# Optimization experiments

Measured on AMD Instinct MI355X. Metric: run time of the kernel, lower is better.

## Reference

```python
import jax, jax.numpy as jnp
import numpy as np

B, S, H, NH = 4, 2048, 1024, 16
HD = H // NH
EPS = 1e-12


def setup_inputs() -> dict:
    key = jax.random.key(0)
    ks = jax.random.split(key, 12)
    sc = 0.02
    return {
        "query": jax.random.normal(ks[0], (B, S, H), dtype=jnp.float32),
        "attention_mask": jnp.zeros((B, 1, 1, S), dtype=jnp.float32),
        "Wq": jax.random.normal(ks[1], (H, H), dtype=jnp.float32) * sc,
        "bq": jnp.zeros((H,), dtype=jnp.float32),
        "Wk": jax.random.normal(ks[2], (H, H), dtype=jnp.float32) * sc,
        "bk": jnp.zeros((H,), dtype=jnp.float32),
        "Wv": jax.random.normal(ks[3], (H, H), dtype=jnp.float32) * sc,
        "bv": jnp.zeros((H,), dtype=jnp.float32),
        "Wd": jax.random.normal(ks[4], (H, H), dtype=jnp.float32) * sc,
        "bd": jnp.zeros((H,), dtype=jnp.float32),
        "ln_gamma": jnp.ones((H,), dtype=jnp.float32),
        "ln_beta": jnp.zeros((H,), dtype=jnp.float32),
    }


def reference(query, attention_mask, Wq, bq, Wk, bk, Wv, bv, Wd, bd, ln_gamma, ln_beta):
    # QKV projections: [B,S,H] -> [B,S,NH,HD]
    q = (query @ Wq + bq).reshape(B, S, NH, HD)
    k = (query @ Wk + bk).reshape(B, S, NH, HD)
    v = (query @ Wv + bv).reshape(B, S, NH, HD)
    # scores: [B,NH,S,S]
    scores = jnp.einsum("bqhd,bkhd->bhqk", q, k) / jnp.sqrt(jnp.float32(HD))
    scores = scores + attention_mask
    probs = jax.nn.softmax(scores, axis=-1)  # attn_dropout p=0 (eval)
    ctx = jnp.einsum("bhqk,bkhd->bqhd", probs, v).reshape(B, S, H)
    hidden = ctx @ Wd + bd  # out_dropout p=0 (eval)
    # pre-LN residual path: LN(hidden) + query
    mu = jnp.mean(hidden, axis=-1, keepdims=True)
    var = jnp.mean(jnp.square(hidden - mu), axis=-1, keepdims=True)
    hidden = (hidden - mu) * jax.lax.rsqrt(var + EPS) * ln_gamma + ln_beta
    return hidden + query
```

## Files before the change

kernel.cpp:

```cpp
#include <hip/hip_runtime.h>
#include <stdint.h>

#define Bn 4
#define Sn 2048
#define Hn 1024
#define NHn 16
#define Mn 8192

typedef unsigned short bf_t;
typedef __attribute__((ext_vector_type(8))) short s16x8;
typedef __attribute__((ext_vector_type(4))) short s16x4;
typedef __attribute__((ext_vector_type(8))) unsigned short u16x8;
typedef __attribute__((ext_vector_type(4))) unsigned short u16x4;
typedef __attribute__((ext_vector_type(4))) float f32x4;
typedef __attribute__((ext_vector_type(4))) unsigned int u32x4;
typedef __attribute__((ext_vector_type(2))) unsigned int u32x2;

__device__ __forceinline__ bf_t f2bf(float f) {
  unsigned int u = __float_as_uint(f);
  u += 0x7fffu + ((u >> 16) & 1u);
  return (bf_t)(u >> 16);
}

__device__ __forceinline__ unsigned pk2(float lo, float hi) {
  return __builtin_amdgcn_perm(__float_as_uint(hi), __float_as_uint(lo), 0x07060302u);
}
__device__ __forceinline__ s16x4 pack4(float a0, float a1, float a2, float a3) {
  u32x2 t;
  t[0] = pk2(a0, a1);
  t[1] = pk2(a2, a3);
  return __builtin_bit_cast(s16x4, t);
}

#define MFMA16K16(a, b, c) __builtin_amdgcn_mfma_f32_16x16x16bf16_1k(a, b, c, 0, 0, 0)
#define MFMA32(a, b, c) __builtin_amdgcn_mfma_f32_16x16x32_bf16(a, b, c, 0, 0, 0)

#define GLOAD16(gp, lp) __builtin_amdgcn_global_load_lds(              \
    (__attribute__((address_space(1))) void*)(gp),                     \
    (__attribute__((address_space(3))) void*)(lp), 16, 0, 0)

__global__ __launch_bounds__(256)
void prep(const float* __restrict__ Wq, const float* __restrict__ Wk,
          const float* __restrict__ Wv, const float* __restrict__ Wd,
          const float* __restrict__ query,
          bf_t* __restrict__ Wt, bf_t* __restrict__ Wdt, bf_t* __restrict__ Xb) {
  __shared__ float tile[32][33];
  const int z = blockIdx.z;
  const int tx = threadIdx.x;
  const int ty = threadIdx.y;
  if (z == 4) {
    const int bid = blockIdx.y * 32 + blockIdx.x;
    const int t = ty * 32 + tx;
    const size_t base = (size_t)bid * 8192 + t * 4;
#pragma unroll
    for (int i = 0; i < 8; i++) {
      const f32x4 v = *(const f32x4*)(query + base + i * 1024);
      u16x4 o;
      o[0] = f2bf(v[0]); o[1] = f2bf(v[1]); o[2] = f2bf(v[2]); o[3] = f2bf(v[3]);
      *(u16x4*)(Xb + base + i * 1024) = o;
    }
    return;
  }
  const float* W = (z == 0) ? Wq : (z == 1) ? Wk : (z == 2) ? Wv : Wd;
  bf_t* dst = (z < 3) ? Wt + (size_t)z * Hn * Hn : Wdt;
  const int n0 = blockIdx.x * 32, k0 = blockIdx.y * 32;
#pragma unroll
  for (int i = 0; i < 4; i++)
    tile[ty + i * 8][tx] = W[(size_t)(k0 + ty + i * 8) * Hn + n0 + tx];
  __syncthreads();
#pragma unroll
  for (int i = 0; i < 4; i++) {
    const int nn = ty + i * 8, kk = tx;
    dst[(size_t)(n0 + nn) * Hn + k0 + kk] = f2bf(tile[kk][nn]);
  }
}

__global__ __launch_bounds__(256, 3)
void gemm_bt(const bf_t* __restrict__ A, const bf_t* __restrict__ Bt,
             const float* __restrict__ b0, const float* __restrict__ b1,
             const float* __restrict__ b2, void* __restrict__ outp,
             int N, int K, int out_bf16)
{
  __shared__ bf_t As[2][4096];
  __shared__ bf_t Bs[2][4096];
  const int tid = threadIdx.x;
  const int wave = tid >> 6, lane = tid & 63;
  const int l15 = lane & 15, quad = lane >> 4;
  const int bm = blockIdx.y * 128, bn = blockIdx.x * 128;
  const int wm = (wave >> 1) * 64, wn = (wave & 1) * 64;
  const int srow = tid >> 2;
  const int scol = (tid & 3) * 8;

  const bf_t* Ag = A + (size_t)(bm + srow) * K + scol;
  const bf_t* Bg = Bt + (size_t)(bn + srow) * K + scol;

  f32x4 acc[4][4] = {};

  GLOAD16(Ag, As[0] + tid * 8);
  GLOAD16(Ag + (size_t)64 * K, As[0] + 2048 + tid * 8);
  GLOAD16(Bg, Bs[0] + tid * 8);
  GLOAD16(Bg + (size_t)64 * K, Bs[0] + 2048 + tid * 8);

  const int nIter = K >> 5;
  for (int i = 0; i < nIter; i++) {
    const int cur = i & 1;
    __syncthreads();
    if (i + 1 < nIter) {
      const int k0 = (i + 1) * 32;
      GLOAD16(Ag + k0, As[cur ^ 1] + tid * 8);
      GLOAD16(Ag + (size_t)64 * K + k0, As[cur ^ 1] + 2048 + tid * 8);
      GLOAD16(Bg + k0, Bs[cur ^ 1] + tid * 8);
      GLOAD16(Bg + (size_t)64 * K + k0, Bs[cur ^ 1] + 2048 + tid * 8);
    }
    s16x8 af[4], bfr[4];
#pragma unroll
    for (int mi = 0; mi < 4; mi++)
      af[mi] = *(const s16x8*)&As[cur][(wm + mi * 16 + l15) * 32 + quad * 8];
#pragma unroll
    for (int ni = 0; ni < 4; ni++)
      bfr[ni] = *(const s16x8*)&Bs[cur][(wn + ni * 16 + l15) * 32 + quad * 8];
#pragma unroll
    for (int mi = 0; mi < 4; mi++)
#pragma unroll
      for (int ni = 0; ni < 4; ni++)
        acc[mi][ni] = __builtin_amdgcn_mfma_f32_16x16x32_bf16(af[mi], bfr[ni], acc[mi][ni], 0, 0, 0);
  }

#pragma unroll
  for (int ni = 0; ni < 4; ni++) {
    const int gn = bn + wn + ni * 16 + l15;
    const float* bp = (gn < 1024) ? b0 : ((gn < 2048) ? b1 : b2);
    const float bias = bp[gn & 1023];
#pragma unroll
    for (int mi = 0; mi < 4; mi++) {
#pragma unroll
      for (int r = 0; r < 4; r++) {
        const int gm = bm + wm + mi * 16 + quad * 4 + r;
        const float v = acc[mi][ni][r] + bias;
        if (out_bf16) ((bf_t*)outp)[(size_t)gm * N + gn] = f2bf(v);
        else          ((float*)outp)[(size_t)gm * N + gn] = v;
      }
    }
  }
}

__global__ __launch_bounds__(256)
void kvswz(const bf_t* __restrict__ qkv, bf_t* __restrict__ Kf,
           bf_t* __restrict__ Vf, const float* __restrict__ mask,
           bf_t* __restrict__ Fb) {
  __shared__ u32x4 smbuf[640];
  const int t = threadIdx.x;
  const int bh = blockIdx.y, b = bh >> 4, h = bh & 15;
  const int k0 = blockIdx.x * 64;

  if (blockIdx.z == 0) {
    bf_t* KT = (bf_t*)smbuf;
#pragma unroll
    for (int i = 0; i < 2; i++) {
      const int c = t + i * 256;
      const int row = c >> 3, col8 = (c & 7) * 8;
      const u16x8 v = *(const u16x8*)(qkv + (size_t)(b * Sn + k0 + row) * 3072 + 1024 + h * 64 + col8);
      *(u16x8*)&KT[row * 80 + col8] = v;
    }
    __syncthreads();
    bf_t* dst0 = Kf + ((size_t)(bh * 32 + blockIdx.x) * 8) * 512;
#pragma unroll
    for (int i = 0; i < 2; i++) {
      const int p = t + i * 256;
      const int frag = p >> 6, lane = p & 63;
      const int ks = frag >> 1, half = frag & 1;
      const int l15 = lane & 15, quad = lane >> 4;
      const u16x8 v = *(const u16x8*)&KT[(ks * 16 + l15) * 80 + half * 32 + quad * 8];
      *(u16x8*)(dst0 + (size_t)frag * 512 + lane * 8) = v;
    }
  } else {
    unsigned int* P32 = (unsigned int*)smbuf;
    {
      const int kp = t >> 3;
      const int d0 = (t & 7) * 8;
      const int kg = k0 + 2 * kp;
      const float f0 = __builtin_amdgcn_exp2f(mask[b * Sn + kg] * 1.44269504f);
      const float f1 = __builtin_amdgcn_exp2f(mask[b * Sn + kg + 1] * 1.44269504f);
      const bf_t* p0 = qkv + (size_t)(b * Sn + kg) * 3072 + 2048 + h * 64 + d0;
      const u16x8 r0 = *(const u16x8*)p0;
      const u16x8 r1 = *(const u16x8*)(p0 + 3072);
#pragma unroll
      for (int j = 0; j < 8; j++) {
        const float v0 = __uint_as_float((unsigned)r0[j] << 16) * f0;
        const float v1 = __uint_as_float((unsigned)r1[j] << 16) * f1;
        P32[(d0 + j) * 33 + kp] = pk2(v0, v1);
      }
    }
    if (h == 0 && t < 64) {
      const float fm = __builtin_amdgcn_exp2f(mask[b * Sn + k0 + t] * 1.44269504f);
      Fb[b * Sn + k0 + t] = f2bf(fm);
    }
    __syncthreads();
    bf_t* dst0 = Vf + ((size_t)(bh * 32 + blockIdx.x) * 8) * 512;
#pragma unroll
    for (int i = 0; i < 2; i++) {
      const int p = t + i * 256;
      const int fp = p >> 6, lane = p & 63;
      const int dvblk = fp >> 1, kpair = fp & 1;
      const int l15 = lane & 15, quad = (lane >> 4) & 3;
      const int d = dvblk * 16 + l15;
      const int c = kpair * 16 + quad * 2;
      u32x4 w;
      w[0] = P32[d * 33 + c];
      w[1] = P32[d * 33 + c + 1];
      w[2] = P32[d * 33 + c + 8];
      w[3] = P32[d * 33 + c + 9];
      *(u32x4*)(dst0 + (size_t)(kpair * 4 + dvblk) * 512 + lane * 8) = w;
    }
  }
}

__global__ __launch_bounds__(512)
void attn(const bf_t* __restrict__ qkv, const bf_t* __restrict__ Kf,
          const bf_t* __restrict__ Vf, const bf_t* __restrict__ Fb,
          bf_t* __restrict__ ctx)
{
  __shared__ __align__(16) bf_t KV[2][2][2][2048];
  __shared__ __align__(16) bf_t Fs[2048];

  const int tid = threadIdx.x;
  const int wave = tid >> 6, lane = tid & 63;
  const int g = wave >> 2, wv = wave & 3;
  const int tg = tid & 255;
  const int l15 = lane & 15, quad = lane >> 4;
  const int idx = blockIdx.x;
  const int bh = idx & 63, b = bh >> 4, h = bh & 15;
  const int q0 = (idx >> 6) * 128;

  if (tid < 256) GLOAD16(Fb + (size_t)b * Sn + tid * 8, Fs + tid * 8);

  s16x8 aq[2][2];
#pragma unroll
  for (int qf = 0; qf < 2; qf++) {
    const bf_t* qp = qkv + (size_t)(b * Sn + q0 + wv * 32 + qf * 16 + l15) * 3072 + h * 64;
    aq[qf][0] = *(const s16x8*)(qp + quad * 8);
    aq[qf][1] = *(const s16x8*)(qp + 32 + quad * 8);
  }

  f32x4 lacc[2] = {};
  f32x4 o[2][4] = {};

  const bf_t* kb = Kf + (size_t)bh * 131072 + (size_t)g * 65536;
  const bf_t* vb = Vf + (size_t)bh * 131072 + (size_t)g * 65536;
  const float C1 = 0.125f * 1.44269504f;

  GLOAD16(kb + tg * 8, KV[g][0][0] + tg * 8);
  GLOAD16(vb + tg * 8, KV[g][1][0] + tg * 8);

  for (int it = 0; it < 32; ++it) {
    const int cur = it & 1;
    __syncthreads();
    if (it < 31) {
      GLOAD16(kb + (it + 1) * 2048 + tg * 8, KV[g][0][cur ^ 1] + tg * 8);
      GLOAD16(vb + (it + 1) * 2048 + tg * 8, KV[g][1][cur ^ 1] + tg * 8);
    }

    s16x4 pb[2][2];
#pragma unroll
    for (int e = 0; e < 2; e++) {
      const s16x8 k0f = *(const s16x8*)&KV[g][0][cur][(e * 2 + 0) * 512 + lane * 8];
      const s16x8 k1f = *(const s16x8*)&KV[g][0][cur][(e * 2 + 1) * 512 + lane * 8];
      const s16x4 ff = *(const s16x4*)&Fs[g * 1024 + it * 32 + e * 16 + quad * 4];
#pragma unroll
      for (int qf = 0; qf < 2; qf++) {
        f32x4 acc = {};
        __builtin_amdgcn_s_setprio(1);
        acc = MFMA32(k0f, aq[qf][0], acc);
        acc = MFMA32(k1f, aq[qf][1], acc);
        __builtin_amdgcn_s_setprio(0);
        const float p0 = __builtin_amdgcn_exp2f(acc[0] * C1);
        const float p1 = __builtin_amdgcn_exp2f(acc[1] * C1);
        const float p2 = __builtin_amdgcn_exp2f(acc[2] * C1);
        const float p3 = __builtin_amdgcn_exp2f(acc[3] * C1);
        pb[qf][e] = pack4(p0, p1, p2, p3);
        lacc[qf] = MFMA16K16(ff, pb[qf][e], lacc[qf]);
      }
    }

    __builtin_amdgcn_s_setprio(1);
#pragma unroll
    for (int dvblk = 0; dvblk < 4; dvblk++) {
      const s16x8 vv = *(const s16x8*)&KV[g][1][cur][dvblk * 512 + lane * 8];
      const s16x4 vlo = {vv[0], vv[1], vv[2], vv[3]};
      const s16x4 vhi = {vv[4], vv[5], vv[6], vv[7]};
#pragma unroll
      for (int qf = 0; qf < 2; qf++) {
        o[qf][dvblk] = MFMA16K16(vlo, pb[qf][0], o[qf][dvblk]);
        o[qf][dvblk] = MFMA16K16(vhi, pb[qf][1], o[qf][dvblk]);
      }
    }
    __builtin_amdgcn_s_setprio(0);
  }

  __syncthreads();
  float* sm = (float*)&KV[0][0][0][0];
  float* sl = (float*)&Fs[0];
  if (g == 1) {
#pragma unroll
    for (int qf = 0; qf < 2; qf++) {
      const int row = wv * 32 + qf * 16 + l15;
#pragma unroll
      for (int dvblk = 0; dvblk < 4; dvblk++) {
        const int col = (dvblk * 16 + quad * 4 + l15 * 4) & 63;
        *(f32x4*)&sm[row * 64 + col] = o[qf][dvblk];
      }
      if (quad == 0) sl[row] = lacc[qf][0];
    }
  }
  __syncthreads();
  if (g == 0) {
#pragma unroll
    for (int qf = 0; qf < 2; qf++) {
      const int row = wv * 32 + qf * 16 + l15;
      const float inv = 1.f / (lacc[qf][0] + sl[row]);
      const size_t grow = (size_t)(b * Sn + q0 + row);
#pragma unroll
      for (int dvblk = 0; dvblk < 4; dvblk++) {
        const int col = (dvblk * 16 + quad * 4 + l15 * 4) & 63;
        const f32x4 o2 = *(const f32x4*)&sm[row * 64 + col];
        u16x4 ov;
#pragma unroll
        for (int r = 0; r < 4; r++) ov[r] = f2bf((o[qf][dvblk][r] + o2[r]) * inv);
        *(u16x4*)&ctx[grow * Hn + h * 64 + dvblk * 16 + quad * 4] = ov;
      }
    }
  }
}

__global__ __launch_bounds__(256)
void ln_res(const float* __restrict__ hid, const float* __restrict__ query,
            const float* __restrict__ gamma, const float* __restrict__ beta,
            float* __restrict__ out)
{
  const int row = blockIdx.x, t = threadIdx.x;
  const f32x4 h = *(const f32x4*)(hid + (size_t)row * Hn + t * 4);
  float s = h[0] + h[1] + h[2] + h[3];
  float ss = h[0]*h[0] + h[1]*h[1] + h[2]*h[2] + h[3]*h[3];
#pragma unroll
  for (int m = 32; m; m >>= 1) { s += __shfl_xor(s, m); ss += __shfl_xor(ss, m); }
  __shared__ float red[8];
  if ((t & 63) == 0) { red[t >> 6] = s; red[4 + (t >> 6)] = ss; }
  __syncthreads();
  s = red[0] + red[1] + red[2] + red[3];
  ss = red[4] + red[5] + red[6] + red[7];
  const float mu = s * (1.f / Hn);
  const float rs = rsqrtf(ss * (1.f / Hn) - mu * mu + 1e-12f);
  const f32x4 q = *(const f32x4*)(query + (size_t)row * Hn + t * 4);
  const f32x4 g = *(const f32x4*)(gamma + t * 4);
  const f32x4 be = *(const f32x4*)(beta + t * 4);
  f32x4 o;
#pragma unroll
  for (int j = 0; j < 4; j++) o[j] = (h[j] - mu) * rs * g[j] + be[j] + q[j];
  *(f32x4*)(out + (size_t)row * Hn + t * 4) = o;
}

extern "C" void kernel_launch(void* const* d_in, const int* in_sizes, int n_in,
                              void* d_out, int out_size, void* d_ws, size_t ws_size,
                              hipStream_t stream) {
  const float* query = (const float*)d_in[0];
  const float* mask  = (const float*)d_in[1];
  const float* Wq = (const float*)d_in[2];
  const float* bq = (const float*)d_in[3];
  const float* Wk = (const float*)d_in[4];
  const float* bk = (const float*)d_in[5];
  const float* Wv = (const float*)d_in[6];
  const float* bv = (const float*)d_in[7];
  const float* Wd = (const float*)d_in[8];
  const float* bd = (const float*)d_in[9];
  const float* gamma = (const float*)d_in[10];
  const float* beta  = (const float*)d_in[11];

  char* w = (char*)d_ws;
  bf_t* Xb  = (bf_t*)w;  w += (size_t)Mn * Hn * 2;
  bf_t* Wt  = (bf_t*)w;  w += (size_t)3 * Hn * Hn * 2;
  bf_t* Wdt = (bf_t*)w;  w += (size_t)Hn * Hn * 2;
  bf_t* QKV = (bf_t*)w;  w += (size_t)Mn * 3 * Hn * 2;
  bf_t* Vf  = (bf_t*)w;  w += (size_t)64 * 32 * 4096 * 2;
  bf_t* Ctx = (bf_t*)w;  w += (size_t)Mn * Hn * 2;
  bf_t* Kf  = (bf_t*)w;
  float* Hid = (float*)w;  w += (size_t)Mn * Hn * 4;
  bf_t* Fb = (bf_t*)w;

  prep<<<dim3(32, 32, 5), dim3(32, 8), 0, stream>>>(Wq, Wk, Wv, Wd, query, Wt, Wdt, Xb);
  gemm_bt<<<dim3(24, 64), 256, 0, stream>>>(Xb, Wt, bq, bk, bv, QKV, 3072, 1024, 1);
  kvswz<<<dim3(32, 64, 2), 256, 0, stream>>>(QKV, Kf, Vf, mask, Fb);
  attn<<<1024, 512, 0, stream>>>(QKV, Kf, Vf, Fb, Ctx);
  gemm_bt<<<dim3(8, 64), 256, 0, stream>>>(Ctx, Wdt, bd, bd, bd, Hid, 1024, 1024, 0);
  ln_res<<<Mn, 256, 0, stream>>>(Hid, query, gamma, beta, (float*)d_out);
}
```

Measured before the change: 331.8 us.

## Load K fragments directly from QKV and double query rows per attention block

```diff
diff --git a/kernel.cpp b/kernel.cpp
--- a/kernel.cpp
+++ b/kernel.cpp
@@ -145,80 +145,55 @@
 }
 
 __global__ __launch_bounds__(256)
-void kvswz(const bf_t* __restrict__ qkv, bf_t* __restrict__ Kf,
-           bf_t* __restrict__ Vf, const float* __restrict__ mask,
-           bf_t* __restrict__ Fb) {
-  __shared__ u32x4 smbuf[640];
+void kvswz(const bf_t* __restrict__ qkv, bf_t* __restrict__ Vf,
+           const float* __restrict__ mask, bf_t* __restrict__ Fb) {
+  __shared__ unsigned int P32[64 * 33];
   const int t = threadIdx.x;
   const int bh = blockIdx.y, b = bh >> 4, h = bh & 15;
   const int k0 = blockIdx.x * 64;
 
-  if (blockIdx.z == 0) {
-    bf_t* KT = (bf_t*)smbuf;
-#pragma unroll
-    for (int i = 0; i < 2; i++) {
-      const int c = t + i * 256;
-      const int row = c >> 3, col8 = (c & 7) * 8;
-      const u16x8 v = *(const u16x8*)(qkv + (size_t)(b * Sn + k0 + row) * 3072 + 1024 + h * 64 + col8);
-      *(u16x8*)&KT[row * 80 + col8] = v;
-    }
-    __syncthreads();
-    bf_t* dst0 = Kf + ((size_t)(bh * 32 + blockIdx.x) * 8) * 512;
-#pragma unroll
-    for (int i = 0; i < 2; i++) {
-      const int p = t + i * 256;
-      const int frag = p >> 6, lane = p & 63;
-      const int ks = frag >> 1, half = frag & 1;
-      const int l15 = lane & 15, quad = lane >> 4;
-      const u16x8 v = *(const u16x8*)&KT[(ks * 16 + l15) * 80 + half * 32 + quad * 8];
-      *(u16x8*)(dst0 + (size_t)frag * 512 + lane * 8) = v;
-    }
-  } else {
-    unsigned int* P32 = (unsigned int*)smbuf;
-    {
-      const int kp = t >> 3;
-      const int d0 = (t & 7) * 8;
-      const int kg = k0 + 2 * kp;
-      const float f0 = __builtin_amdgcn_exp2f(mask[b * Sn + kg] * 1.44269504f);
-      const float f1 = __builtin_amdgcn_exp2f(mask[b * Sn + kg + 1] * 1.44269504f);
-      const bf_t* p0 = qkv + (size_t)(b * Sn + kg) * 3072 + 2048 + h * 64 + d0;
-      const u16x8 r0 = *(const u16x8*)p0;
-      const u16x8 r1 = *(const u16x8*)(p0 + 3072);
-#pragma unroll
-      for (int j = 0; j < 8; j++) {
-        const float v0 = __uint_as_float((unsigned)r0[j] << 16) * f0;
-        const float v1 = __uint_as_float((unsigned)r1[j] << 16) * f1;
-        P32[(d0 + j) * 33 + kp] = pk2(v0, v1);
-      }
-    }
-    if (h == 0 && t < 64) {
-      const float fm = __builtin_amdgcn_exp2f(mask[b * Sn + k0 + t] * 1.44269504f);
-      Fb[b * Sn + k0 + t] = f2bf(fm);
-    }
-    __syncthreads();
-    bf_t* dst0 = Vf + ((size_t)(bh * 32 + blockIdx.x) * 8) * 512;
-#pragma unroll
-    for (int i = 0; i < 2; i++) {
-      const int p = t + i * 256;
-      const int fp = p >> 6, lane = p & 63;
-      const int dvblk = fp >> 1, kpair = fp & 1;
-      const int l15 = lane & 15, quad = (lane >> 4) & 3;
-      const int d = dvblk * 16 + l15;
-      const int c = kpair * 16 + quad * 2;
-      u32x4 w;
-      w[0] = P32[d * 33 + c];
-      w[1] = P32[d * 33 + c + 1];
-      w[2] = P32[d * 33 + c + 8];
-      w[3] = P32[d * 33 + c + 9];
-      *(u32x4*)(dst0 + (size_t)(kpair * 4 + dvblk) * 512 + lane * 8) = w;
-    }
+  {
+    const int kp = t >> 3;
+    const int d0 = (t & 7) * 8;
+    const int kg = k0 + 2 * kp;
+    const float f0 = __builtin_amdgcn_exp2f(mask[b * Sn + kg] * 1.44269504f);
+    const float f1 = __builtin_amdgcn_exp2f(mask[b * Sn + kg + 1] * 1.44269504f);
+    const bf_t* p0 = qkv + (size_t)(b * Sn + kg) * 3072 + 2048 + h * 64 + d0;
+    const u16x8 r0 = *(const u16x8*)p0;
+    const u16x8 r1 = *(const u16x8*)(p0 + 3072);
+#pragma unroll
+    for (int j = 0; j < 8; j++) {
+      const float v0 = __uint_as_float((unsigned)r0[j] << 16) * f0;
+      const float v1 = __uint_as_float((unsigned)r1[j] << 16) * f1;
+      P32[(d0 + j) * 33 + kp] = pk2(v0, v1);
+    }
+  }
+  if (h == 0 && t < 64) {
+    const float fm = __builtin_amdgcn_exp2f(mask[b * Sn + k0 + t] * 1.44269504f);
+    Fb[b * Sn + k0 + t] = f2bf(fm);
+  }
+  __syncthreads();
+  bf_t* dst0 = Vf + ((size_t)(bh * 32 + blockIdx.x) * 8) * 512;
+#pragma unroll
+  for (int i = 0; i < 2; i++) {
+    const int p = t + i * 256;
+    const int fp = p >> 6, lane = p & 63;
+    const int dvblk = fp >> 1, kpair = fp & 1;
+    const int l15 = lane & 15, quad = (lane >> 4) & 3;
+    const int d = dvblk * 16 + l15;
+    const int c = kpair * 16 + quad * 2;
+    u32x4 w;
+    w[0] = P32[d * 33 + c];
+    w[1] = P32[d * 33 + c + 1];
+    w[2] = P32[d * 33 + c + 8];
+    w[3] = P32[d * 33 + c + 9];
+    *(u32x4*)(dst0 + (size_t)(kpair * 4 + dvblk) * 512 + lane * 8) = w;
   }
 }
 
 __global__ __launch_bounds__(512)
-void attn(const bf_t* __restrict__ qkv, const bf_t* __restrict__ Kf,
-          const bf_t* __restrict__ Vf, const bf_t* __restrict__ Fb,
-          bf_t* __restrict__ ctx)
+void attn(const bf_t* __restrict__ qkv, const bf_t* __restrict__ Vf,
+          const bf_t* __restrict__ Fb, bf_t* __restrict__ ctx)
 {
   __shared__ __align__(16) bf_t KV[2][2][2][2048];
   __shared__ __align__(16) bf_t Fs[2048];
@@ -230,44 +205,47 @@
   const int l15 = lane & 15, quad = lane >> 4;
   const int idx = blockIdx.x;
   const int bh = idx & 63, b = bh >> 4, h = bh & 15;
-  const int q0 = (idx >> 6) * 128;
+  const int q0 = (idx >> 6) * 256;
 
   if (tid < 256) GLOAD16(Fb + (size_t)b * Sn + tid * 8, Fs + tid * 8);
 
-  s16x8 aq[2][2];
-#pragma unroll
-  for (int qf = 0; qf < 2; qf++) {
-    const bf_t* qp = qkv + (size_t)(b * Sn + q0 + wv * 32 + qf * 16 + l15) * 3072 + h * 64;
+  s16x8 aq[4][2];
+#pragma unroll
+  for (int qf = 0; qf < 4; qf++) {
+    const bf_t* qp = qkv + (size_t)(b * Sn + q0 + wv * 64 + qf * 16 + l15) * 3072 + h * 64;
     aq[qf][0] = *(const s16x8*)(qp + quad * 8);
     aq[qf][1] = *(const s16x8*)(qp + 32 + quad * 8);
   }
 
-  f32x4 lacc[2] = {};
-  f32x4 o[2][4] = {};
-
-  const bf_t* kb = Kf + (size_t)bh * 131072 + (size_t)g * 65536;
+  f32x4 lacc[4] = {};
+  f32x4 o[4][4] = {};
+
+  const int ks = tg >> 7, kh = (tg >> 6) & 1;
+  const int lg = tg & 63, l15g = lg & 15, quadg = lg >> 4;
+  const bf_t* kq = qkv + (size_t)(b * Sn + g * 1024 + ks * 16 + l15g) * 3072
+                   + 1024 + h * 64 + kh * 32 + quadg * 8;
   const bf_t* vb = Vf + (size_t)bh * 131072 + (size_t)g * 65536;
   const float C1 = 0.125f * 1.44269504f;
 
-  GLOAD16(kb + tg * 8, KV[g][0][0] + tg * 8);
+  GLOAD16(kq, KV[g][0][0] + tg * 8);
   GLOAD16(vb + tg * 8, KV[g][1][0] + tg * 8);
 
   for (int it = 0; it < 32; ++it) {
     const int cur = it & 1;
     __syncthreads();
     if (it < 31) {
-      GLOAD16(kb + (it + 1) * 2048 + tg * 8, KV[g][0][cur ^ 1] + tg * 8);
+      GLOAD16(kq + (size_t)(it + 1) * 98304, KV[g][0][cur ^ 1] + tg * 8);
       GLOAD16(vb + (it + 1) * 2048 + tg * 8, KV[g][1][cur ^ 1] + tg * 8);
     }
 
-    s16x4 pb[2][2];
+    s16x4 pb[4][2];
 #pragma unroll
     for (int e = 0; e < 2; e++) {
       const s16x8 k0f = *(const s16x8*)&KV[g][0][cur][(e * 2 + 0) * 512 + lane * 8];
       const s16x8 k1f = *(const s16x8*)&KV[g][0][cur][(e * 2 + 1) * 512 + lane * 8];
       const s16x4 ff = *(const s16x4*)&Fs[g * 1024 + it * 32 + e * 16 + quad * 4];
 #pragma unroll
-      for (int qf = 0; qf < 2; qf++) {
+      for (int qf = 0; qf < 4; qf++) {
         f32x4 acc = {};
         __builtin_amdgcn_s_setprio(1);
         acc = MFMA32(k0f, aq[qf][0], acc);
@@ -289,7 +267,7 @@
       const s16x4 vlo = {vv[0], vv[1], vv[2], vv[3]};
       const s16x4 vhi = {vv[4], vv[5], vv[6], vv[7]};
 #pragma unroll
-      for (int qf = 0; qf < 2; qf++) {
+      for (int qf = 0; qf < 4; qf++) {
         o[qf][dvblk] = MFMA16K16(vlo, pb[qf][0], o[qf][dvblk]);
         o[qf][dvblk] = MFMA16K16(vhi, pb[qf][1], o[qf][dvblk]);
       }
@@ -297,36 +275,41 @@
     __builtin_amdgcn_s_setprio(0);
   }
 
-  __syncthreads();
   float* sm = (float*)&KV[0][0][0][0];
   float* sl = (float*)&Fs[0];
-  if (g == 1) {
-#pragma unroll
-    for (int qf = 0; qf < 2; qf++) {
-      const int row = wv * 32 + qf * 16 + l15;
-#pragma unroll
-      for (int dvblk = 0; dvblk < 4; dvblk++) {
-        const int col = (dvblk * 16 + quad * 4 + l15 * 4) & 63;
-        *(f32x4*)&sm[row * 64 + col] = o[qf][dvblk];
-      }
-      if (quad == 0) sl[row] = lacc[qf][0];
-    }
-  }
-  __syncthreads();
-  if (g == 0) {
-#pragma unroll
-    for (int qf = 0; qf < 2; qf++) {
-      const int row = wv * 32 + qf * 16 + l15;
-      const float inv = 1.f / (lacc[qf][0] + sl[row]);
-      const size_t grow = (size_t)(b * Sn + q0 + row);
-#pragma unroll
-      for (int dvblk = 0; dvblk < 4; dvblk++) {
-        const int col = (dvblk * 16 + quad * 4 + l15 * 4) & 63;
-        const f32x4 o2 = *(const f32x4*)&sm[row * 64 + col];
-        u16x4 ov;
-#pragma unroll
-        for (int r = 0; r < 4; r++) ov[r] = f2bf((o[qf][dvblk][r] + o2[r]) * inv);
-        *(u16x4*)&ctx[grow * Hn + h * 64 + dvblk * 16 + quad * 4] = ov;
+#pragma unroll
+  for (int qh = 0; qh < 2; qh++) {
+    __syncthreads();
+    if (g == 1) {
+#pragma unroll
+      for (int lq = 0; lq < 2; lq++) {
+        const int qf = qh * 2 + lq;
+        const int rp = wv * 32 + lq * 16 + l15;
+#pragma unroll
+        for (int dvblk = 0; dvblk < 4; dvblk++) {
+          const int col = (dvblk * 16 + quad * 4 + l15 * 4) & 63;
+          *(f32x4*)&sm[rp * 64 + col] = o[qf][dvblk];
+        }
+        if (quad == 0) sl[rp] = lacc[qf][0];
+      }
+    }
+    __syncthreads();
+    if (g == 0) {
+#pragma unroll
+      for (int lq = 0; lq < 2; lq++) {
+        const int qf = qh * 2 + lq;
+        const int rp = wv * 32 + lq * 16 + l15;
+        const float inv = 1.f / (lacc[qf][0] + sl[rp]);
+        const size_t grow = (size_t)(b * Sn + q0 + wv * 64 + qf * 16 + l15);
+#pragma unroll
+        for (int dvblk = 0; dvblk < 4; dvblk++) {
+          const int col = (dvblk * 16 + quad * 4 + l15 * 4) & 63;
+          const f32x4 o2 = *(const f32x4*)&sm[rp * 64 + col];
+          u16x4 ov;
+#pragma unroll
+          for (int r = 0; r < 4; r++) ov[r] = f2bf((o[qf][dvblk][r] + o2[r]) * inv);
+          *(u16x4*)&ctx[grow * Hn + h * 64 + dvblk * 16 + quad * 4] = ov;
+        }
       }
     }
   }
@@ -382,14 +365,13 @@
   bf_t* QKV = (bf_t*)w;  w += (size_t)Mn * 3 * Hn * 2;
   bf_t* Vf  = (bf_t*)w;  w += (size_t)64 * 32 * 4096 * 2;
   bf_t* Ctx = (bf_t*)w;  w += (size_t)Mn * Hn * 2;
-  bf_t* Kf  = (bf_t*)w;
   float* Hid = (float*)w;  w += (size_t)Mn * Hn * 4;
   bf_t* Fb = (bf_t*)w;
 
   prep<<<dim3(32, 32, 5), dim3(32, 8), 0, stream>>>(Wq, Wk, Wv, Wd, query, Wt, Wdt, Xb);
   gemm_bt<<<dim3(24, 64), 256, 0, stream>>>(Xb, Wt, bq, bk, bv, QKV, 3072, 1024, 1);
-  kvswz<<<dim3(32, 64, 2), 256, 0, stream>>>(QKV, Kf, Vf, mask, Fb);
-  attn<<<1024, 512, 0, stream>>>(QKV, Kf, Vf, Fb, Ctx);
+  kvswz<<<dim3(32, 64), 256, 0, stream>>>(QKV, Vf, mask, Fb);
+  attn<<<512, 512, 0, stream>>>(QKV, Vf, Fb, Ctx);
   gemm_bt<<<dim3(8, 64), 256, 0, stream>>>(Ctx, Wdt, bd, bd, bd, Hid, 1024, 1024, 0);
   ln_res<<<Mn, 256, 0, stream>>>(Hid, query, gamma, beta, (float*)d_out);
 }
```

New measurement: 357.0 us. 7.6% more time.

## Double attention block to 256 queries and remap GEMM workgroups across XCDs

Applied to the files above, without the earlier changes.

```diff
diff --git a/kernel.cpp b/kernel.cpp
--- a/kernel.cpp
+++ b/kernel.cpp
@@ -86,7 +86,14 @@
   const int tid = threadIdx.x;
   const int wave = tid >> 6, lane = tid & 63;
   const int l15 = lane & 15, quad = lane >> 4;
-  const int bm = blockIdx.y * 128, bn = blockIdx.x * 128;
+
+  const int nwg = gridDim.x * gridDim.y;
+  const int lin = blockIdx.y * gridDim.x + blockIdx.x;
+  const int qc = nwg >> 3;
+  const int wg = (lin & 7) * qc + (lin >> 3);
+  const int bxs = wg % gridDim.x, bys = wg / gridDim.x;
+  const int bm = bys * 128, bn = bxs * 128;
+
   const int wm = (wave >> 1) * 64, wn = (wave & 1) * 64;
   const int srow = tid >> 2;
   const int scol = (tid & 3) * 8;
@@ -215,7 +222,7 @@
   }
 }
 
-__global__ __launch_bounds__(512)
+__global__ __launch_bounds__(1024)
 void attn(const bf_t* __restrict__ qkv, const bf_t* __restrict__ Kf,
           const bf_t* __restrict__ Vf, const bf_t* __restrict__ Fb,
           bf_t* __restrict__ ctx)
@@ -225,12 +232,12 @@
 
   const int tid = threadIdx.x;
   const int wave = tid >> 6, lane = tid & 63;
-  const int g = wave >> 2, wv = wave & 3;
-  const int tg = tid & 255;
+  const int g = wave >> 3, wv = wave & 7;
+  const int tg = tid & 511;
   const int l15 = lane & 15, quad = lane >> 4;
   const int idx = blockIdx.x;
   const int bh = idx & 63, b = bh >> 4, h = bh & 15;
-  const int q0 = (idx >> 6) * 128;
+  const int q0 = (idx >> 6) * 256;
 
   if (tid < 256) GLOAD16(Fb + (size_t)b * Sn + tid * 8, Fs + tid * 8);
 
@@ -249,15 +256,17 @@
   const bf_t* vb = Vf + (size_t)bh * 131072 + (size_t)g * 65536;
   const float C1 = 0.125f * 1.44269504f;
 
-  GLOAD16(kb + tg * 8, KV[g][0][0] + tg * 8);
-  GLOAD16(vb + tg * 8, KV[g][1][0] + tg * 8);
+  if (tg < 256) GLOAD16(kb + tg * 8, KV[g][0][0] + tg * 8);
+  else          GLOAD16(vb + (tg - 256) * 8, KV[g][1][0] + (tg - 256) * 8);
 
   for (int it = 0; it < 32; ++it) {
     const int cur = it & 1;
     __syncthreads();
     if (it < 31) {
-      GLOAD16(kb + (it + 1) * 2048 + tg * 8, KV[g][0][cur ^ 1] + tg * 8);
-      GLOAD16(vb + (it + 1) * 2048 + tg * 8, KV[g][1][cur ^ 1] + tg * 8);
+      if (tg < 256)
+        GLOAD16(kb + (it + 1) * 2048 + tg * 8, KV[g][0][cur ^ 1] + tg * 8);
+      else
+        GLOAD16(vb + (it + 1) * 2048 + (tg - 256) * 8, KV[g][1][cur ^ 1] + (tg - 256) * 8);
     }
 
     s16x4 pb[2][2];
@@ -297,36 +306,39 @@
     __builtin_amdgcn_s_setprio(0);
   }
 
-  __syncthreads();
   float* sm = (float*)&KV[0][0][0][0];
   float* sl = (float*)&Fs[0];
-  if (g == 1) {
-#pragma unroll
-    for (int qf = 0; qf < 2; qf++) {
-      const int row = wv * 32 + qf * 16 + l15;
-#pragma unroll
-      for (int dvblk = 0; dvblk < 4; dvblk++) {
-        const int col = (dvblk * 16 + quad * 4 + l15 * 4) & 63;
-        *(f32x4*)&sm[row * 64 + col] = o[qf][dvblk];
-      }
-      if (quad == 0) sl[row] = lacc[qf][0];
-    }
-  }
-  __syncthreads();
-  if (g == 0) {
-#pragma unroll
-    for (int qf = 0; qf < 2; qf++) {
-      const int row = wv * 32 + qf * 16 + l15;
-      const float inv = 1.f / (lacc[qf][0] + sl[row]);
-      const size_t grow = (size_t)(b * Sn + q0 + row);
-#pragma unroll
-      for (int dvblk = 0; dvblk < 4; dvblk++) {
-        const int col = (dvblk * 16 + quad * 4 + l15 * 4) & 63;
-        const f32x4 o2 = *(const f32x4*)&sm[row * 64 + col];
-        u16x4 ov;
-#pragma unroll
-        for (int r = 0; r < 4; r++) ov[r] = f2bf((o[qf][dvblk][r] + o2[r]) * inv);
-        *(u16x4*)&ctx[grow * Hn + h * 64 + dvblk * 16 + quad * 4] = ov;
+#pragma unroll
+  for (int ph = 0; ph < 2; ph++) {
+    __syncthreads();
+    if (g == 1 && (wv >> 2) == ph) {
+#pragma unroll
+      for (int qf = 0; qf < 2; qf++) {
+        const int rp = (wv & 3) * 32 + qf * 16 + l15;
+#pragma unroll
+        for (int dvblk = 0; dvblk < 4; dvblk++) {
+          const int col = (dvblk * 16 + quad * 4 + l15 * 4) & 63;
+          *(f32x4*)&sm[rp * 64 + col] = o[qf][dvblk];
+        }
+        if (quad == 0) sl[rp] = lacc[qf][0];
+      }
+    }
+    __syncthreads();
+    if (g == 0 && (wv >> 2) == ph) {
+#pragma unroll
+      for (int qf = 0; qf < 2; qf++) {
+        const int rp = (wv & 3) * 32 + qf * 16 + l15;
+        const float inv = 1.f / (lacc[qf][0] + sl[rp]);
+        const size_t grow = (size_t)(b * Sn + q0 + wv * 32 + qf * 16 + l15);
+#pragma unroll
+        for (int dvblk = 0; dvblk < 4; dvblk++) {
+          const int col = (dvblk * 16 + quad * 4 + l15 * 4) & 63;
+          const f32x4 o2 = *(const f32x4*)&sm[rp * 64 + col];
+          u16x4 ov;
+#pragma unroll
+          for (int r = 0; r < 4; r++) ov[r] = f2bf((o[qf][dvblk][r] + o2[r]) * inv);
+          *(u16x4*)&ctx[grow * Hn + h * 64 + dvblk * 16 + quad * 4] = ov;
+        }
       }
     }
   }
@@ -389,7 +401,7 @@
   prep<<<dim3(32, 32, 5), dim3(32, 8), 0, stream>>>(Wq, Wk, Wv, Wd, query, Wt, Wdt, Xb);
   gemm_bt<<<dim3(24, 64), 256, 0, stream>>>(Xb, Wt, bq, bk, bv, QKV, 3072, 1024, 1);
   kvswz<<<dim3(32, 64, 2), 256, 0, stream>>>(QKV, Kf, Vf, mask, Fb);
-  attn<<<1024, 512, 0, stream>>>(QKV, Kf, Vf, Fb, Ctx);
+  attn<<<512, 1024, 0, stream>>>(QKV, Kf, Vf, Fb, Ctx);
   gemm_bt<<<dim3(8, 64), 256, 0, stream>>>(Ctx, Wdt, bd, bd, bd, Hid, 1024, 1024, 0);
   ln_res<<<Mn, 256, 0, stream>>>(Hid, query, gamma, beta, (float*)d_out);
 }
```

After: 328.8 us. Within noise of the previous version (-0.9%).

## Fuse K/V swizzle into QKV GEMM epilogue and remap workgroups

Applied to the files above, without the earlier changes.

```diff
diff --git a/kernel.cpp b/kernel.cpp
--- a/kernel.cpp
+++ b/kernel.cpp
@@ -42,8 +42,9 @@
 __global__ __launch_bounds__(256)
 void prep(const float* __restrict__ Wq, const float* __restrict__ Wk,
           const float* __restrict__ Wv, const float* __restrict__ Wd,
-          const float* __restrict__ query,
-          bf_t* __restrict__ Wt, bf_t* __restrict__ Wdt, bf_t* __restrict__ Xb) {
+          const float* __restrict__ query, const float* __restrict__ mask,
+          bf_t* __restrict__ Wt, bf_t* __restrict__ Wdt, bf_t* __restrict__ Xb,
+          bf_t* __restrict__ Fb) {
   __shared__ float tile[32][33];
   const int z = blockIdx.z;
   const int tx = threadIdx.x;
@@ -59,6 +60,13 @@
       o[0] = f2bf(v[0]); o[1] = f2bf(v[1]); o[2] = f2bf(v[2]); o[3] = f2bf(v[3]);
       *(u16x4*)(Xb + base + i * 1024) = o;
     }
+    if (bid < 4) {
+#pragma unroll
+      for (int i = 0; i < 8; i++) {
+        const int s = t * 8 + i;
+        Fb[bid * Sn + s] = f2bf(__builtin_amdgcn_exp2f(mask[(size_t)bid * Sn + s] * 1.44269504f));
+      }
+    }
     return;
   }
   const float* W = (z == 0) ? Wq : (z == 1) ? Wk : (z == 2) ? Wv : Wd;
@@ -79,14 +87,25 @@
 void gemm_bt(const bf_t* __restrict__ A, const bf_t* __restrict__ Bt,
              const float* __restrict__ b0, const float* __restrict__ b1,
              const float* __restrict__ b2, void* __restrict__ outp,
-             int N, int K, int out_bf16)
+             int N, int K, int out_bf16,
+             const float* __restrict__ mask, bf_t* __restrict__ Kf,
+             bf_t* __restrict__ Vf, int fuse_kv)
 {
-  __shared__ bf_t As[2][4096];
-  __shared__ bf_t Bs[2][4096];
+  __shared__ __align__(16) char smem[33536];
+  bf_t (*As)[4096] = (bf_t(*)[4096])smem;
+  bf_t (*Bs)[4096] = (bf_t(*)[4096])(smem + 16384);
+
   const int tid = threadIdx.x;
   const int wave = tid >> 6, lane = tid & 63;
   const int l15 = lane & 15, quad = lane >> 4;
-  const int bm = blockIdx.y * 128, bn = blockIdx.x * 128;
+
+  const int nwg = gridDim.x * gridDim.y;
+  const int lin = blockIdx.y * gridDim.x + blockIdx.x;
+  const int qc = nwg >> 3;
+  const int wg = (lin & 7) * qc + (lin >> 3);
+  const int bxs = wg % gridDim.x, bys = wg / gridDim.x;
+  const int bm = bys * 128, bn = bxs * 128;
+
   const int wm = (wave >> 1) * 64, wn = (wave & 1) * 64;
   const int srow = tid >> 2;
   const int scol = (tid & 3) * 8;
@@ -126,91 +145,86 @@
         acc[mi][ni] = __builtin_amdgcn_mfma_f32_16x16x32_bf16(af[mi], bfr[ni], acc[mi][ni], 0, 0, 0);
   }
 
-#pragma unroll
-  for (int ni = 0; ni < 4; ni++) {
-    const int gn = bn + wn + ni * 16 + l15;
-    const float* bp = (gn < 1024) ? b0 : ((gn < 2048) ? b1 : b2);
-    const float bias = bp[gn & 1023];
-#pragma unroll
-    for (int mi = 0; mi < 4; mi++) {
+  if (!fuse_kv || bn < 1024) {
+#pragma unroll
+    for (int ni = 0; ni < 4; ni++) {
+      const int gn = bn + wn + ni * 16 + l15;
+      const float* bp = (gn < 1024) ? b0 : ((gn < 2048) ? b1 : b2);
+      const float bias = bp[gn & 1023];
+#pragma unroll
+      for (int mi = 0; mi < 4; mi++) {
+#pragma unroll
+        for (int r = 0; r < 4; r++) {
+          const int gm = bm + wm + mi * 16 + quad * 4 + r;
+          const float v = acc[mi][ni][r] + bias;
+          if (out_bf16) ((bf_t*)outp)[(size_t)gm * N + gn] = f2bf(v);
+          else          ((float*)outp)[(size_t)gm * N + gn] = v;
+        }
+      }
+    }
+  } else if (bn < 2048) {
+    const int bb = bm >> 11, k0b = bm & 2047;
+#pragma unroll
+    for (int ni = 0; ni < 4; ni++) {
+      const int dK = (bn - 1024) + wn + ni * 16 + l15;
+      const int h = dK >> 6, d = dK & 63;
+      const float bias = b1[dK];
+      const int half = d >> 5, qo = (d >> 3) & 3, j = d & 7;
+      const size_t hb = (size_t)((bb * 16 + h) * 32) * 8 * 512;
+#pragma unroll
+      for (int mi = 0; mi < 4; mi++) {
+#pragma unroll
+        for (int r = 0; r < 4; r++) {
+          const int kk = k0b + wm + mi * 16 + quad * 4 + r;
+          const int chunk = kk >> 6, ks = (kk >> 4) & 3, l15o = kk & 15;
+          Kf[hb + ((size_t)chunk * 8 + ks * 2 + half) * 512 + (qo * 16 + l15o) * 8 + j]
+            = f2bf(acc[mi][ni][r] + bias);
+        }
+      }
+    }
+  } else {
+    __syncthreads();
+    unsigned* VP = (unsigned*)smem;
+    const int bb = bm >> 11, k0b = bm & 2047;
+    float fv[4][4];
+#pragma unroll
+    for (int mi = 0; mi < 4; mi++)
 #pragma unroll
       for (int r = 0; r < 4; r++) {
-        const int gm = bm + wm + mi * 16 + quad * 4 + r;
-        const float v = acc[mi][ni][r] + bias;
-        if (out_bf16) ((bf_t*)outp)[(size_t)gm * N + gn] = f2bf(v);
-        else          ((float*)outp)[(size_t)gm * N + gn] = v;
-      }
-    }
-  }
-}
-
-__global__ __launch_bounds__(256)
-void kvswz(const bf_t* __restrict__ qkv, bf_t* __restrict__ Kf,
-           bf_t* __restrict__ Vf, const float* __restrict__ mask,
-           bf_t* __restrict__ Fb) {
-  __shared__ u32x4 smbuf[640];
-  const int t = threadIdx.x;
-  const int bh = blockIdx.y, b = bh >> 4, h = bh & 15;
-  const int k0 = blockIdx.x * 64;
-
-  if (blockIdx.z == 0) {
-    bf_t* KT = (bf_t*)smbuf;
-#pragma unroll
-    for (int i = 0; i < 2; i++) {
-      const int c = t + i * 256;
-      const int row = c >> 3, col8 = (c & 7) * 8;
-      const u16x8 v = *(const u16x8*)(qkv + (size_t)(b * Sn + k0 + row) * 3072 + 1024 + h * 64 + col8);
-      *(u16x8*)&KT[row * 80 + col8] = v;
+        const int kk = k0b + wm + mi * 16 + quad * 4 + r;
+        fv[mi][r] = __builtin_amdgcn_exp2f(mask[(size_t)bb * Sn + kk] * 1.44269504f);
+      }
+#pragma unroll
+    for (int ni = 0; ni < 4; ni++) {
+      const int lc = wn + ni * 16 + l15;
+      const float bias = b2[(bn - 2048) + lc];
+#pragma unroll
+      for (int mi = 0; mi < 4; mi++) {
+#pragma unroll
+        for (int rp = 0; rp < 2; rp++) {
+          const int lr = wm + mi * 16 + quad * 4 + rp * 2;
+          const float v0 = __uint_as_float((unsigned)f2bf(acc[mi][ni][rp * 2]     + bias) << 16) * fv[mi][rp * 2];
+          const float v1 = __uint_as_float((unsigned)f2bf(acc[mi][ni][rp * 2 + 1] + bias) << 16) * fv[mi][rp * 2 + 1];
+          VP[lc * 65 + (lr >> 1)] = pk2(v0, v1);
+        }
+      }
     }
     __syncthreads();
-    bf_t* dst0 = Kf + ((size_t)(bh * 32 + blockIdx.x) * 8) * 512;
-#pragma unroll
-    for (int i = 0; i < 2; i++) {
-      const int p = t + i * 256;
-      const int frag = p >> 6, lane = p & 63;
-      const int ks = frag >> 1, half = frag & 1;
-      const int l15 = lane & 15, quad = lane >> 4;
-      const u16x8 v = *(const u16x8*)&KT[(ks * 16 + l15) * 80 + half * 32 + quad * 8];
-      *(u16x8*)(dst0 + (size_t)frag * 512 + lane * 8) = v;
-    }
-  } else {
-    unsigned int* P32 = (unsigned int*)smbuf;
-    {
-      const int kp = t >> 3;
-      const int d0 = (t & 7) * 8;
-      const int kg = k0 + 2 * kp;
-      const float f0 = __builtin_amdgcn_exp2f(mask[b * Sn + kg] * 1.44269504f);
-      const float f1 = __builtin_amdgcn_exp2f(mask[b * Sn + kg + 1] * 1.44269504f);
-      const bf_t* p0 = qkv + (size_t)(b * Sn + kg) * 3072 + 2048 + h * 64 + d0;
-      const u16x8 r0 = *(const u16x8*)p0;
-      const u16x8 r1 = *(const u16x8*)(p0 + 3072);
-#pragma unroll
-      for (int j = 0; j < 8; j++) {
-        const float v0 = __uint_as_float((unsigned)r0[j] << 16) * f0;
-        const float v1 = __uint_as_float((unsigned)r1[j] << 16) * f1;
-        P32[(d0 + j) * 33 + kp] = pk2(v0, v1);
-      }
-    }
-    if (h == 0 && t < 64) {
-      const float fm = __builtin_amdgcn_exp2f(mask[b * Sn + k0 + t] * 1.44269504f);
-      Fb[b * Sn + k0 + t] = f2bf(fm);
-    }
-    __syncthreads();
-    bf_t* dst0 = Vf + ((size_t)(bh * 32 + blockIdx.x) * 8) * 512;
-#pragma unroll
-    for (int i = 0; i < 2; i++) {
-      const int p = t + i * 256;
-      const int fp = p >> 6, lane = p & 63;
-      const int dvblk = fp >> 1, kpair = fp & 1;
-      const int l15 = lane & 15, quad = (lane >> 4) & 3;
-      const int d = dvblk * 16 + l15;
-      const int c = kpair * 16 + quad * 2;
+    const int hbase = (bn - 2048) >> 6;
+#pragma unroll
+    for (int i = 0; i < 8; i++) {
+      const int p = tid + i * 256;
+      const int unit = p >> 9, fp = (p >> 6) & 7, ln2 = p & 63;
+      const int uh = unit & 1, uc = unit >> 1;
+      const int kpair = fp >> 2, dvb = fp & 3;
+      const int l15o = ln2 & 15, qo = ln2 >> 4;
+      const int lc = uh * 64 + dvb * 16 + l15o;
+      const int kp = uc * 32 + kpair * 16 + qo * 2;
       u32x4 w;
-      w[0] = P32[d * 33 + c];
-      w[1] = P32[d * 33 + c + 1];
-      w[2] = P32[d * 33 + c + 8];
-      w[3] = P32[d * 33 + c + 9];
-      *(u32x4*)(dst0 + (size_t)(kpair * 4 + dvblk) * 512 + lane * 8) = w;
+      w[0] = VP[lc * 65 + kp];     w[1] = VP[lc * 65 + kp + 1];
+      w[2] = VP[lc * 65 + kp + 8]; w[3] = VP[lc * 65 + kp + 9];
+      const int bh = bb * 16 + hbase + uh, chunk = (k0b >> 6) + uc;
+      *(u32x4*)(Vf + ((size_t)(bh * 32 + chunk) * 8 + fp) * 512 + ln2 * 8) = w;
     }
   }
 }
@@ -386,10 +400,11 @@
   float* Hid = (float*)w;  w += (size_t)Mn * Hn * 4;
   bf_t* Fb = (bf_t*)w;
 
-  prep<<<dim3(32, 32, 5), dim3(32, 8), 0, stream>>>(Wq, Wk, Wv, Wd, query, Wt, Wdt, Xb);
-  gemm_bt<<<dim3(24, 64), 256, 0, stream>>>(Xb, Wt, bq, bk, bv, QKV, 3072, 1024, 1);
-  kvswz<<<dim3(32, 64, 2), 256, 0, stream>>>(QKV, Kf, Vf, mask, Fb);
+  prep<<<dim3(32, 32, 5), dim3(32, 8), 0, stream>>>(Wq, Wk, Wv, Wd, query, mask, Wt, Wdt, Xb, Fb);
+  gemm_bt<<<dim3(24, 64), 256, 0, stream>>>(Xb, Wt, bq, bk, bv, QKV, 3072, 1024, 1,
+                                            mask, Kf, Vf, 1);
   attn<<<1024, 512, 0, stream>>>(QKV, Kf, Vf, Fb, Ctx);
-  gemm_bt<<<dim3(8, 64), 256, 0, stream>>>(Ctx, Wdt, bd, bd, bd, Hid, 1024, 1024, 0);
+  gemm_bt<<<dim3(8, 64), 256, 0, stream>>>(Ctx, Wdt, bd, bd, bd, Hid, 1024, 1024, 0,
+                                           nullptr, nullptr, nullptr, 0);
   ln_res<<<Mn, 256, 0, stream>>>(Hid, query, gamma, beta, (float*)d_out);
 }
```

New measurement: 307.4 us. -7.4%, faster.
